# Kernel optimization log

Measured on AMD Instinct MI355X. Metric: run time of the kernel, lower is better.

Reference implementation:

```python
import jax, jax.numpy as jnp
import numpy as np
import math

D_MODEL = 1024
NUM_HEADS = 16
D_HEAD = D_MODEL // NUM_HEADS          # 64
N_FREQ = D_HEAD // 2 + 1               # 33 rfft bins
COMPRESSION_RATIO = 0.5


def setup_inputs() -> dict:
    key = jax.random.key(0)
    k_x, k_qkv, k_out, k_b, k_m = jax.random.split(key, 5)
    B, S = 2, 2048
    x = jax.random.normal(k_x, (B, S, D_MODEL), dtype=jnp.float32)
    # Linear weights stored as [in, out] (torch Linear uses [out, in]; math identical).
    w_qkv = jax.random.normal(k_qkv, (D_MODEL, 3 * D_MODEL), dtype=jnp.float32) / math.sqrt(D_MODEL)
    w_out = jax.random.normal(k_out, (D_MODEL, D_MODEL), dtype=jnp.float32) / math.sqrt(D_MODEL)
    b_out = jax.random.normal(k_b, (D_MODEL,), dtype=jnp.float32) * 0.01
    # Learned per-frequency-bin mask logits of AdaptiveFrequencyMask(d_state=d_head).
    # Initialized around logit(compression_ratio) with small noise.
    init_logit = math.log(COMPRESSION_RATIO / (1.0 - COMPRESSION_RATIO))
    mask_logits = init_logit + 0.1 * jax.random.normal(k_m, (N_FREQ,), dtype=jnp.float32)
    return {"x": x, "w_qkv": w_qkv, "w_out": w_out, "b_out": b_out, "mask_logits": mask_logits}


def _spectral_filter(t, mask):
    # rfft over d_head dim, apply learned soft mask, inverse rfft.  t: [B,H,S,dh]
    tf = jnp.fft.rfft(t, axis=-1)          # [B,H,S,N_FREQ] complex
    tf = tf * mask                          # broadcast real mask over bins
    return jnp.fft.irfft(tf, n=t.shape[-1], axis=-1).astype(t.dtype)


def reference(x, w_qkv, w_out, b_out, mask_logits):
    B, S, D = x.shape
    H, dh = NUM_HEADS, D_HEAD
    qkv = x @ w_qkv                                         # [B,S,3D]
    q, k, v = jnp.split(qkv, 3, axis=-1)
    # [B,S,D] -> [B,H,S,dh]
    to_heads = lambda t: t.reshape(B, S, H, dh).transpose(0, 2, 1, 3)
    q, k, v = to_heads(q), to_heads(k), to_heads(v)
    mask = jax.nn.sigmoid(mask_logits)                      # [N_FREQ]
    q = _spectral_filter(q, mask)
    k = _spectral_filter(k, mask)
    scores = jnp.einsum('bhqd,bhkd->bhqk', q, k) / math.sqrt(dh)
    attn = jax.nn.softmax(scores, axis=-1)                  # dropout p=0 (eval)
    out = jnp.einsum('bhqk,bhkd->bhqd', attn, v)
    out = out.transpose(0, 2, 1, 3).reshape(B, S, D)
    return out @ w_out + b_out
```

## Files before the change

### kernel.cpp

```cpp
#include <hip/hip_runtime.h>

#define S_LEN 2048
#define NH    16
#define DH    64
#define DM    1024
#define NQKV  3072

typedef __attribute__((ext_vector_type(8))) __bf16 bf16x8;
typedef __attribute__((ext_vector_type(4))) float  f32x4;
typedef unsigned short ushort_t;

static __device__ __forceinline__ unsigned short bf16b(float f) {
  return __builtin_bit_cast(unsigned short, (__bf16)f);
}

static __device__ __forceinline__ float exp2v(float x) {
  return __builtin_amdgcn_exp2f(x);
}

static __device__ __forceinline__ bf16x8 pack8(float4 f0, float4 f1) {
  uint4 v;
  v.x = ((unsigned)bf16b(f0.y) << 16) | bf16b(f0.x);
  v.y = ((unsigned)bf16b(f0.w) << 16) | bf16b(f0.z);
  v.z = ((unsigned)bf16b(f1.y) << 16) | bf16b(f1.x);
  v.w = ((unsigned)bf16b(f1.w) << 16) | bf16b(f1.z);
  return __builtin_bit_cast(bf16x8, v);
}

static __device__ __forceinline__ void glds16(const void* g, void* l) {
  __builtin_amdgcn_global_load_lds((const __attribute__((address_space(1))) unsigned int*)g,
                                   (__attribute__((address_space(3))) unsigned int*)l, 16, 0, 0);
}

#define OFF_WT  65536ull
#define OFF_WOT 6356992ull
#define OFF_Q   8454144ull
#define OFF_K   16842752ull
#define OFF_V   25231360ull
#define OFF_AO  33619968ull

__global__ __launch_bounds__(256) void k_prep(const float* __restrict__ wqkv,
                                              const float* __restrict__ wout,
                                              const float* __restrict__ x,
                                              const float* __restrict__ logits,
                                              unsigned short* __restrict__ Wt,
                                              unsigned short* __restrict__ Wot,
                                              unsigned short* __restrict__ xb) {
  __shared__ __align__(16) char sbuf[16640];
  int bid = blockIdx.x;
  int t = threadIdx.x;

  if (bid < 256) {
    float* msk = (float*)sbuf;
    float* Kd  = (float*)(sbuf + 144);
    ushort_t (*Fb)[72] = (ushort_t(*)[72])(sbuf + 416);
    if (t < 33) msk[t] = 1.0f / (1.0f + __expf(-logits[t]));
    __syncthreads();
    if (t < 64) {
      float acc = msk[0];
      #pragma unroll
      for (int f = 1; f < 32; ++f) {
        int r = (f * t) & 63;
        acc += 2.0f * msk[f] * __cosf((float)r * (6.28318530717958647692f / 64.0f));
      }
      acc += msk[32] * ((t & 1) ? -1.0f : 1.0f);
      Kd[t] = acc * (1.0f / 64.0f);
    }
    __syncthreads();
    for (int idx = t; idx < 4096; idx += 256) {
      int j = idx >> 6, i = idx & 63;
      Fb[j][i] = bf16b(Kd[(j - i) & 63]);
    }
    __syncthreads();

    int lane = t & 63, w = t >> 6;
    int m16 = lane & 15, quad = lane >> 4;
    int kx = bid >> 5, yy = bid & 31;
    int which = yy >> 4, h = yy & 15;
    int base = which * 1024 + h * 64;

    bf16x8 af0 = *(const bf16x8*)(&Fb[w * 16 + m16][quad * 8]);
    bf16x8 af1 = *(const bf16x8*)(&Fb[w * 16 + m16][32 + quad * 8]);

    f32x4 acc[8] = {};
    #pragma unroll 2
    for (int n = 0; n < 8; ++n) {
      const float* Wg = wqkv + (size_t)(kx * 128 + n * 16 + m16) * NQKV + base + quad * 8;
      float4 a0 = *(const float4*)(Wg);
      float4 a1 = *(const float4*)(Wg + 4);
      float4 b0 = *(const float4*)(Wg + 32);
      float4 b1 = *(const float4*)(Wg + 36);
      acc[n] = __builtin_amdgcn_mfma_f32_16x16x32_bf16(af0, pack8(a0, a1), acc[n], 0, 0, 0);
      acc[n] = __builtin_amdgcn_mfma_f32_16x16x32_bf16(af1, pack8(b0, b1), acc[n], 0, 0, 0);
    }
    float sc = (which == 0) ? 0.18033688011112042f : 1.0f;
    #pragma unroll
    for (int n = 0; n < 8; ++n) {
      #pragma unroll
      for (int r = 0; r < 4; ++r) {
        int j = w * 16 + quad * 4 + r;
        Wt[(size_t)(base + j) * DM + kx * 128 + n * 16 + m16] = bf16b(acc[n][r] * sc);
      }
    }
  } else if (bid < 768) {
    float (*Ts)[65] = (float(*)[65])sbuf;
    int b1 = bid - 256;
    if (b1 < 256) {
      int kt = b1 & 15, nt = b1 >> 4;
      int cb = 2048 + nt * 64, kbase = kt * 64;
      #pragma unroll
      for (int p = 0; p < 16; ++p) {
        int kk = p * 4 + (t >> 6);
        Ts[kk][t & 63] = wqkv[(size_t)(kbase + kk) * NQKV + cb + (t & 63)];
      }
      __syncthreads();
      #pragma unroll
      for (int p = 0; p < 16; ++p) {
        int nn = p * 4 + (t >> 6);
        Wt[(size_t)(cb + nn) * DM + kbase + (t & 63)] = bf16b(Ts[t & 63][nn]);
      }
    } else {
      int b2 = b1 - 256;
      int kt = b2 & 15, nt = b2 >> 4;
      int cb = nt * 64, kbase = kt * 64;
      #pragma unroll
      for (int p = 0; p < 16; ++p) {
        int kk = p * 4 + (t >> 6);
        Ts[kk][t & 63] = wout[(size_t)(kbase + kk) * DM + cb + (t & 63)];
      }
      __syncthreads();
      #pragma unroll
      for (int p = 0; p < 16; ++p) {
        int nn = p * 4 + (t >> 6);
        Wot[(size_t)(cb + nn) * DM + kbase + (t & 63)] = bf16b(Ts[t & 63][nn]);
      }
    }
  } else {
    size_t i = ((size_t)(bid - 768) * 256 + t) * 8;
    const float4* xp = (const float4*)(x + i);
    float4 a = xp[0], b = xp[1];
    uint4 v;
    v.x = ((unsigned)bf16b(a.y) << 16) | bf16b(a.x);
    v.y = ((unsigned)bf16b(a.w) << 16) | bf16b(a.z);
    v.z = ((unsigned)bf16b(b.y) << 16) | bf16b(b.x);
    v.w = ((unsigned)bf16b(b.w) << 16) | bf16b(b.z);
    *(uint4*)(xb + i) = v;
  }
}

__device__ __forceinline__ void gemm_core_async(const unsigned short* __restrict__ A,
                                                const unsigned short* __restrict__ Bw,
                                                int bm, int bn, unsigned short* smem,
                                                f32x4 (&acc)[4][4]) {
  unsigned short* As = smem;
  unsigned short* Bs = smem + 8192;
  int t = threadIdx.x, lane = t & 63, w = t >> 6;
  int m16 = lane & 15, quad = lane >> 4;
  int wr = (w >> 1) * 64, wc = (w & 1) * 64;
  int lr = lane >> 3, lc = lane & 7;
  int gc = lc ^ lr;
  int xr = m16 & 7;
  const unsigned short* Agb = A  + (size_t)(bm * 128) * DM + gc * 8;
  const unsigned short* Bgb = Bw + (size_t)(bn * 128) * DM + gc * 8;

  for (int k0 = 0; k0 < DM; k0 += 64) {
    #pragma unroll
    for (int p = 0; p < 4; ++p) {
      int row = p * 32 + w * 8 + lr;
      glds16(Agb + (size_t)row * DM + k0, As + row * 64 + lc * 8);
      glds16(Bgb + (size_t)row * DM + k0, Bs + row * 64 + lc * 8);
    }
    __syncthreads();
    #pragma unroll
    for (int kk = 0; kk < 2; ++kk) {
      bf16x8 af[4], bfr[4];
      #pragma unroll
      for (int i = 0; i < 4; ++i)
        af[i] = *(const bf16x8*)(As + (wr + i * 16 + m16) * 64 + ((kk * 4 + quad) ^ xr) * 8);
      #pragma unroll
      for (int j = 0; j < 4; ++j)
        bfr[j] = *(const bf16x8*)(Bs + (wc + j * 16 + m16) * 64 + ((kk * 4 + quad) ^ xr) * 8);
      #pragma unroll
      for (int i = 0; i < 4; ++i)
        #pragma unroll
        for (int j = 0; j < 4; ++j)
          acc[i][j] = __builtin_amdgcn_mfma_f32_16x16x32_bf16(af[i], bfr[j], acc[i][j], 0, 0, 0);
    }
    __syncthreads();
  }
}

__global__ __launch_bounds__(256) void k_gemm_qkv(const unsigned short* __restrict__ xb,
                                                  const unsigned short* __restrict__ Bw,
                                                  unsigned short* __restrict__ Qb,
                                                  unsigned short* __restrict__ Kb,
                                                  unsigned short* __restrict__ Vt) {
  __shared__ __align__(16) unsigned short smem[18432];
  f32x4 acc[4][4] = {};
  int bn = blockIdx.x, bm = blockIdx.y;
  gemm_core_async(xb, Bw, bm, bn, smem, acc);

  int t = threadIdx.x, lane = t & 63, w = t >> 6;
  int m16 = lane & 15, quad = lane >> 4;
  int wr = (w >> 1) * 64, wc = (w & 1) * 64;
  int b = bm >> 4, srow = (bm & 15) * 128;
  int which = bn >> 3;
  ushort_t (*Tr)[130] = (ushort_t(*)[130])smem;
  if (which < 2) {
    #pragma unroll
    for (int i = 0; i < 4; ++i)
      #pragma unroll
      for (int j = 0; j < 4; ++j)
        #pragma unroll
        for (int r = 0; r < 4; ++r)
          Tr[wr + i * 16 + quad * 4 + r][wc + j * 16 + m16] = bf16b(acc[i][j][r]);
    __syncthreads();
    int row = t >> 1, half = t & 1;
    int cloc = bn * 128 + half * 64 - which * 1024;
    int h = cloc >> 6;
    unsigned short* dst = (which ? Kb : Qb) +
        ((size_t)(b * 16 + h) * 2048 + srow + row) * 64;
    #pragma unroll
    for (int p = 0; p < 8; ++p)
      *(uint4*)(dst + p * 8) = *(const uint4*)(&Tr[row][half * 64 + p * 8]);
  } else {
    #pragma unroll
    for (int i = 0; i < 4; ++i)
      #pragma unroll
      for (int j = 0; j < 4; ++j)
        #pragma unroll
        for (int r = 0; r < 4; ++r)
          Tr[wc + j * 16 + m16][wr + i * 16 + quad * 4 + r] = bf16b(acc[i][j][r]);
    __syncthreads();
    int dl = t >> 1, half = t & 1;
    int cloc = (bn - 16) * 128 + dl;
    int h = cloc >> 6, d = cloc & 63;
    unsigned short* dst = Vt + ((size_t)(b * 16 + h) * 64 + d) * 2048 + srow + half * 64;
    #pragma unroll
    for (int p = 0; p < 8; ++p)
      *(uint4*)(dst + p * 8) = *(const uint4*)(&Tr[dl][half * 64 + p * 8]);
  }
}

__global__ __launch_bounds__(512, 4) void k_attn(const unsigned short* __restrict__ Qb,
                                                 const unsigned short* __restrict__ Kb,
                                                 const unsigned short* __restrict__ Vt,
                                                 unsigned short* __restrict__ AO) {
  __shared__ __align__(16) unsigned short smem[33280];
  int t = threadIdx.x;
  int w = t >> 6, lane = t & 63;
  int m16 = lane & 15, quad = lane >> 4;
  int bid = blockIdx.x;
  int jj = bid >> 3;
  int bh = ((jj & 3) << 3) + (bid & 7);
  int qbase = (jj >> 2) * 128 + w * 16;

  const unsigned short* Qp = Qb + ((size_t)bh * S_LEN + qbase + m16) * DH + quad * 8;
  bf16x8 aq0 = *(const bf16x8*)(Qp);
  bf16x8 aq1 = *(const bf16x8*)(Qp + 32);
  const unsigned short* Kbase = Kb + (size_t)bh * S_LEN * DH;
  const unsigned short* Vbase = Vt + (size_t)bh * DH * S_LEN;

  unsigned short* Pw = smem + 24576 + w * 1088;
  int xr = m16 & 7;

  int trow = t >> 3;
  int tcol = t & 7;
  int gswz = tcol ^ (trow & 7);
  const unsigned short* Kg = Kbase + (size_t)trow * 64 + gswz * 8;
  const unsigned short* Vg = Vbase + (size_t)trow * S_LEN + gswz * 8;
  unsigned short* Kl = smem + trow * 64 + tcol * 8;
  unsigned short* Vl = smem + 12288 + trow * 64 + tcol * 8;

  f32x4 o[4] = {};
  float l = 0.f;
  f32x4 zero = {0.f, 0.f, 0.f, 0.f};

  glds16(Kg,        Kl);
  glds16(Vg,        Vl);
  glds16(Kg + 4096, Kl + 4096);
  glds16(Vg + 64,   Vl + 4096);

  int buf = 0, slot = 2;
  #pragma unroll 1
  for (int kt = 0; kt < S_LEN / 64; ++kt) {
    if (kt + 1 < S_LEN / 64) asm volatile("s_waitcnt vmcnt(2)" ::: "memory");
    else                     asm volatile("s_waitcnt vmcnt(0)" ::: "memory");
    __builtin_amdgcn_s_barrier();
    __builtin_amdgcn_sched_barrier(0);
    if (kt + 2 < S_LEN / 64) {
      glds16(Kg + (size_t)(kt + 2) * 4096, Kl + slot * 4096);
      glds16(Vg + (kt + 2) * 64,           Vl + slot * 4096);
    }
    unsigned short* Ksh = smem + buf * 4096;
    unsigned short* Vsh = smem + 12288 + buf * 4096;

    f32x4 st[4];
    __builtin_amdgcn_s_setprio(1);
    #pragma unroll
    for (int g = 0; g < 4; ++g) {
      int rk = g * 16 + m16;
      bf16x8 kf0 = *(const bf16x8*)(Ksh + rk * 64 + ((quad ^ xr) * 8));
      bf16x8 kf1 = *(const bf16x8*)(Ksh + rk * 64 + (((4 + quad) ^ xr) * 8));
      st[g] = __builtin_amdgcn_mfma_f32_16x16x32_bf16(kf0, aq0, zero, 0, 0, 0);
      st[g] = __builtin_amdgcn_mfma_f32_16x16x32_bf16(kf1, aq1, st[g], 0, 0, 0);
    }
    __builtin_amdgcn_s_setprio(0);
    #pragma unroll
    for (int g = 0; g < 4; ++g) {
      float p0 = exp2v(st[g][0]), p1 = exp2v(st[g][1]);
      float p2 = exp2v(st[g][2]), p3 = exp2v(st[g][3]);
      l += (p0 + p1) + (p2 + p3);
      uint2 pk;
      pk.x = ((unsigned)bf16b(p1) << 16) | bf16b(p0);
      pk.y = ((unsigned)bf16b(p3) << 16) | bf16b(p2);
      *(uint2*)(Pw + m16 * 68 + g * 16 + quad * 4) = pk;
    }
    __builtin_amdgcn_s_setprio(1);
    #pragma unroll
    for (int c = 0; c < 2; ++c) {
      bf16x8 ap = *(const bf16x8*)(Pw + m16 * 68 + c * 32 + quad * 8);
      #pragma unroll
      for (int j = 0; j < 4; ++j) {
        int dv = j * 16 + m16;
        bf16x8 bv = *(const bf16x8*)(Vsh + dv * 64 + (((c * 4 + quad) ^ xr) * 8));
        o[j] = __builtin_amdgcn_mfma_f32_16x16x32_bf16(ap, bv, o[j], 0, 0, 0);
      }
    }
    __builtin_amdgcn_s_setprio(0);
    buf  = (buf  == 2) ? 0 : buf  + 1;
    slot = (slot == 2) ? 0 : slot + 1;
  }

  l += __shfl_xor(l, 16); l += __shfl_xor(l, 32);
  float iv = 1.0f / l;
  int b = bh >> 4, h = bh & 15;
  #pragma unroll
  for (int r = 0; r < 4; ++r) {
    float v0 = __shfl(iv, quad * 4 + r);
    size_t row0 = (size_t)b * S_LEN + qbase + quad * 4 + r;
    unsigned short* d0 = AO + row0 * DM + h * DH + m16;
    #pragma unroll
    for (int j = 0; j < 4; ++j)
      d0[j * 16] = bf16b(o[j][r] * v0);
  }
}

__global__ __launch_bounds__(256) void k_gemm_out(const unsigned short* __restrict__ A,
                                                  const unsigned short* __restrict__ Bw,
                                                  const float* __restrict__ bias,
                                                  float* __restrict__ out) {
  __shared__ __align__(16) unsigned short smem[18432];
  f32x4 acc[4][4] = {};
  int bn = blockIdx.x, bm = blockIdx.y;
  gemm_core_async(A, Bw, bm, bn, smem, acc);

  int t = threadIdx.x, lane = t & 63, w = t >> 6;
  int m16 = lane & 15, quad = lane >> 4;
  int wr = (w >> 1) * 64, wc = (w & 1) * 64;
  #pragma unroll
  for (int i = 0; i < 4; ++i) {
    int grow = bm * 128 + wr + i * 16 + quad * 4;
    #pragma unroll
    for (int j = 0; j < 4; ++j) {
      int gc = bn * 128 + wc + j * 16 + m16;
      float bb = bias[gc];
      #pragma unroll
      for (int r = 0; r < 4; ++r)
        out[(size_t)(grow + r) * DM + gc] = acc[i][j][r] + bb;
    }
  }
}

extern "C" void kernel_launch(void* const* d_in, const int* in_sizes, int n_in,
                              void* d_out, int out_size, void* d_ws, size_t ws_size,
                              hipStream_t stream) {
  const float* x    = (const float*)d_in[0];
  const float* wqkv = (const float*)d_in[1];
  const float* wout = (const float*)d_in[2];
  const float* bout = (const float*)d_in[3];
  const float* mlog = (const float*)d_in[4];
  char* ws = (char*)d_ws;
  unsigned short* Wt  = (unsigned short*)(ws + OFF_WT);
  unsigned short* Wot = (unsigned short*)(ws + OFF_WOT);
  unsigned short* Qb  = (unsigned short*)(ws + OFF_Q);
  unsigned short* Kb  = (unsigned short*)(ws + OFF_K);
  unsigned short* Vt  = (unsigned short*)(ws + OFF_V);
  unsigned short* xb  = (unsigned short*)(ws + OFF_AO);
  unsigned short* AO  = (unsigned short*)(ws + OFF_AO);
  float* out = (float*)d_out;

  k_prep<<<dim3(2816), dim3(256), 0, stream>>>(wqkv, wout, x, mlog, Wt, Wot, xb);
  k_gemm_qkv<<<dim3(24, 32), dim3(256), 0, stream>>>(xb, Wt, Qb, Kb, Vt);
  k_attn<<<dim3(512), dim3(512), 0, stream>>>(Qb, Kb, Vt, AO);
  k_gemm_out<<<dim3(8, 32), dim3(256), 0, stream>>>(AO, Wot, bout, out);
}
```

Measured before the change: 215.5 us.

## Process two 16-row query tiles per wave in attention kernel

Each wave in the attention kernel now computes 32 query rows (two 16-row MFMA tiles) instead of 16. Every K/V fragment read from shared memory feeds twice as many MFMAs, and global K/V traffic per query is halved. The grid shrinks from 512 to 256 blocks and the launch-bounds occupancy hint drops from 4 to 2. The trade-off is more accumulator registers, a larger P buffer, and fewer resident blocks per CU to hide memory latency.

Result: no change. 218.8 us (+1.5%).

```diff
diff --git a/kernel.cpp b/kernel.cpp
--- a/kernel.cpp
+++ b/kernel.cpp
@@ -242,26 +242,29 @@
   }
 }
 
-__global__ __launch_bounds__(512, 4) void k_attn(const unsigned short* __restrict__ Qb,
+__global__ __launch_bounds__(512, 2) void k_attn(const unsigned short* __restrict__ Qb,
                                                  const unsigned short* __restrict__ Kb,
                                                  const unsigned short* __restrict__ Vt,
                                                  unsigned short* __restrict__ AO) {
-  __shared__ __align__(16) unsigned short smem[33280];
+  __shared__ __align__(16) unsigned short smem[41984];
   int t = threadIdx.x;
   int w = t >> 6, lane = t & 63;
   int m16 = lane & 15, quad = lane >> 4;
   int bid = blockIdx.x;
   int jj = bid >> 3;
   int bh = ((jj & 3) << 3) + (bid & 7);
-  int qbase = (jj >> 2) * 128 + w * 16;
-
-  const unsigned short* Qp = Qb + ((size_t)bh * S_LEN + qbase + m16) * DH + quad * 8;
-  bf16x8 aq0 = *(const bf16x8*)(Qp);
-  bf16x8 aq1 = *(const bf16x8*)(Qp + 32);
+  int qbase = (jj >> 2) * 256 + w * 32;
+
+  const unsigned short* QpA = Qb + ((size_t)bh * S_LEN + qbase + m16) * DH + quad * 8;
+  const unsigned short* QpB = QpA + 16 * DH;
+  bf16x8 aq0A = *(const bf16x8*)(QpA);
+  bf16x8 aq1A = *(const bf16x8*)(QpA + 32);
+  bf16x8 aq0B = *(const bf16x8*)(QpB);
+  bf16x8 aq1B = *(const bf16x8*)(QpB + 32);
   const unsigned short* Kbase = Kb + (size_t)bh * S_LEN * DH;
   const unsigned short* Vbase = Vt + (size_t)bh * DH * S_LEN;
 
-  unsigned short* Pw = smem + 24576 + w * 1088;
+  unsigned short* Pw = smem + 24576 + w * 2176;
   int xr = m16 & 7;
 
   int trow = t >> 3;
@@ -272,8 +275,8 @@
   unsigned short* Kl = smem + trow * 64 + tcol * 8;
   unsigned short* Vl = smem + 12288 + trow * 64 + tcol * 8;
 
-  f32x4 o[4] = {};
-  float l = 0.f;
+  f32x4 oA[4] = {}, oB[4] = {};
+  float lA = 0.f, lB = 0.f;
   f32x4 zero = {0.f, 0.f, 0.f, 0.f};
 
   glds16(Kg,        Kl);
@@ -295,36 +298,47 @@
     unsigned short* Ksh = smem + buf * 4096;
     unsigned short* Vsh = smem + 12288 + buf * 4096;
 
-    f32x4 st[4];
+    f32x4 stA[4], stB[4];
     __builtin_amdgcn_s_setprio(1);
     #pragma unroll
     for (int g = 0; g < 4; ++g) {
       int rk = g * 16 + m16;
       bf16x8 kf0 = *(const bf16x8*)(Ksh + rk * 64 + ((quad ^ xr) * 8));
       bf16x8 kf1 = *(const bf16x8*)(Ksh + rk * 64 + (((4 + quad) ^ xr) * 8));
-      st[g] = __builtin_amdgcn_mfma_f32_16x16x32_bf16(kf0, aq0, zero, 0, 0, 0);
-      st[g] = __builtin_amdgcn_mfma_f32_16x16x32_bf16(kf1, aq1, st[g], 0, 0, 0);
+      stA[g] = __builtin_amdgcn_mfma_f32_16x16x32_bf16(kf0, aq0A, zero, 0, 0, 0);
+      stA[g] = __builtin_amdgcn_mfma_f32_16x16x32_bf16(kf1, aq1A, stA[g], 0, 0, 0);
+      stB[g] = __builtin_amdgcn_mfma_f32_16x16x32_bf16(kf0, aq0B, zero, 0, 0, 0);
+      stB[g] = __builtin_amdgcn_mfma_f32_16x16x32_bf16(kf1, aq1B, stB[g], 0, 0, 0);
     }
     __builtin_amdgcn_s_setprio(0);
     #pragma unroll
     for (int g = 0; g < 4; ++g) {
-      float p0 = exp2v(st[g][0]), p1 = exp2v(st[g][1]);
-      float p2 = exp2v(st[g][2]), p3 = exp2v(st[g][3]);
-      l += (p0 + p1) + (p2 + p3);
-      uint2 pk;
-      pk.x = ((unsigned)bf16b(p1) << 16) | bf16b(p0);
-      pk.y = ((unsigned)bf16b(p3) << 16) | bf16b(p2);
-      *(uint2*)(Pw + m16 * 68 + g * 16 + quad * 4) = pk;
+      float a0 = exp2v(stA[g][0]), a1 = exp2v(stA[g][1]);
+      float a2 = exp2v(stA[g][2]), a3 = exp2v(stA[g][3]);
+      lA += (a0 + a1) + (a2 + a3);
+      uint2 pka;
+      pka.x = ((unsigned)bf16b(a1) << 16) | bf16b(a0);
+      pka.y = ((unsigned)bf16b(a3) << 16) | bf16b(a2);
+      *(uint2*)(Pw + m16 * 68 + g * 16 + quad * 4) = pka;
+      float b0 = exp2v(stB[g][0]), b1 = exp2v(stB[g][1]);
+      float b2 = exp2v(stB[g][2]), b3 = exp2v(stB[g][3]);
+      lB += (b0 + b1) + (b2 + b3);
+      uint2 pkb;
+      pkb.x = ((unsigned)bf16b(b1) << 16) | bf16b(b0);
+      pkb.y = ((unsigned)bf16b(b3) << 16) | bf16b(b2);
+      *(uint2*)(Pw + (16 + m16) * 68 + g * 16 + quad * 4) = pkb;
     }
     __builtin_amdgcn_s_setprio(1);
     #pragma unroll
     for (int c = 0; c < 2; ++c) {
-      bf16x8 ap = *(const bf16x8*)(Pw + m16 * 68 + c * 32 + quad * 8);
+      bf16x8 apA = *(const bf16x8*)(Pw + m16 * 68 + c * 32 + quad * 8);
+      bf16x8 apB = *(const bf16x8*)(Pw + (16 + m16) * 68 + c * 32 + quad * 8);
       #pragma unroll
       for (int j = 0; j < 4; ++j) {
         int dv = j * 16 + m16;
         bf16x8 bv = *(const bf16x8*)(Vsh + dv * 64 + (((c * 4 + quad) ^ xr) * 8));
-        o[j] = __builtin_amdgcn_mfma_f32_16x16x32_bf16(ap, bv, o[j], 0, 0, 0);
+        oA[j] = __builtin_amdgcn_mfma_f32_16x16x32_bf16(apA, bv, oA[j], 0, 0, 0);
+        oB[j] = __builtin_amdgcn_mfma_f32_16x16x32_bf16(apB, bv, oB[j], 0, 0, 0);
       }
     }
     __builtin_amdgcn_s_setprio(0);
@@ -332,17 +346,23 @@
     slot = (slot == 2) ? 0 : slot + 1;
   }
 
-  l += __shfl_xor(l, 16); l += __shfl_xor(l, 32);
-  float iv = 1.0f / l;
+  lA += __shfl_xor(lA, 16); lA += __shfl_xor(lA, 32);
+  lB += __shfl_xor(lB, 16); lB += __shfl_xor(lB, 32);
+  float ivA = 1.0f / lA;
+  float ivB = 1.0f / lB;
   int b = bh >> 4, h = bh & 15;
   #pragma unroll
   for (int r = 0; r < 4; ++r) {
-    float v0 = __shfl(iv, quad * 4 + r);
+    float vA = __shfl(ivA, quad * 4 + r);
+    float vB = __shfl(ivB, quad * 4 + r);
     size_t row0 = (size_t)b * S_LEN + qbase + quad * 4 + r;
     unsigned short* d0 = AO + row0 * DM + h * DH + m16;
-    #pragma unroll
-    for (int j = 0; j < 4; ++j)
-      d0[j * 16] = bf16b(o[j][r] * v0);
+    unsigned short* d1 = AO + (row0 + 16) * DM + h * DH + m16;
+    #pragma unroll
+    for (int j = 0; j < 4; ++j) {
+      d0[j * 16] = bf16b(oA[j][r] * vA);
+      d1[j * 16] = bf16b(oB[j][r] * vB);
+    }
   }
 }
 
@@ -392,6 +412,6 @@
 
   k_prep<<<dim3(2816), dim3(256), 0, stream>>>(wqkv, wout, x, mlog, Wt, Wot, xb);
   k_gemm_qkv<<<dim3(24, 32), dim3(256), 0, stream>>>(xb, Wt, Qb, Kb, Vt);
-  k_attn<<<dim3(512), dim3(512), 0, stream>>>(Qb, Kb, Vt, AO);
+  k_attn<<<dim3(256), dim3(512), 0, stream>>>(Qb, Kb, Vt, AO);
   k_gemm_out<<<dim3(8, 32), dim3(256), 0, stream>>>(AO, Wot, bout, out);
 }
```
